# Kernel optimization log

Hardware: AMD Instinct MI355X
Metric: run time of the kernel (lower is better)

The kernel has to match this reference:

```python
import jax, jax.numpy as jnp
import numpy as np

B, C, H, W = 4, 64, 64, 64
K = C // 8  # conv_f / conv_g output channels (scale=8 since C>=8)


def setup_inputs() -> dict:
    key = jax.random.key(0)
    ks = jax.random.split(key, 8)
    x = jax.random.normal(ks[0], (B, C, H, W), dtype=jnp.float32)
    Wf = jax.random.normal(ks[1], (K, C), dtype=jnp.float32) * 0.05
    bf = jnp.zeros((K,), dtype=jnp.float32)
    Wg = jax.random.normal(ks[2], (K, C), dtype=jnp.float32) * 0.05
    bg = jnp.zeros((K,), dtype=jnp.float32)
    Wh = jax.random.normal(ks[3], (C, C), dtype=jnp.float32) * 0.05
    bh = jnp.zeros((C,), dtype=jnp.float32)
    gamma = jax.random.uniform(ks[4], (1,), dtype=jnp.float32)
    return {"x": x, "Wf": Wf, "bf": bf, "Wg": Wg, "bg": bg,
            "Wh": Wh, "bh": bh, "gamma": gamma}


def reference(x, Wf, bf, Wg, bg, Wh, bh, gamma):
    Bn, Cn, Hn, Wn = x.shape
    HW = Hn * Wn
    xf = x.reshape(Bn, Cn, HW)                               # [B, C, HW]
    # 1x1 convs == per-pixel linear maps over channels
    f = jnp.einsum('kc,bcn->bkn', Wf, xf) + bf[None, :, None]  # [B, K, HW]
    g = jnp.einsum('kc,bcn->bkn', Wg, xf) + bg[None, :, None]  # [B, K, HW]
    h = jnp.einsum('dc,bcn->bdn', Wh, xf) + bh[None, :, None]  # [B, C, HW]
    # s = f^T @ g  -> [B, HW, HW]
    s = jnp.einsum('bki,bkj->bij', f, g)
    # softmax over dim=1 (the first HW axis), matching F.softmax(s, dim=1)
    b = jax.nn.softmax(s, axis=1)
    # post-softmax lower-triangular mask applied to b^T (lower_tri=True)
    tri = jnp.tril(jnp.ones((HW, HW), dtype=x.dtype))
    b_masked = jnp.swapaxes(b, 1, 2) * tri                   # [B, HW, HW]
    o = jnp.einsum('bcn,bnm->bcm', h, b_masked)              # [B, C, HW]
    y = (gamma[0] * o + xf).reshape(Bn, Cn, Hn, Wn)
    return y
```

## Files before the change

kernel.cpp:

```cpp
#include <hip/hip_runtime.h>
#include <hip/hip_bf16.h>

#define HW 4096
#define CC 64
#define NB 4

typedef short bf16x8 __attribute__((ext_vector_type(8)));
typedef float f32x4 __attribute__((ext_vector_type(4)));

#define OFF_F  0
#define OFF_G  262144
#define OFF_H  524288
#define OFF_ZI 2621440
#define OFF_O  2686976

__device__ __forceinline__ float bf2f(short s) {
    unsigned u = ((unsigned)(unsigned short)s) << 16;
    return __uint_as_float(u);
}

__global__ __launch_bounds__(256) void k_prep(
    const float* __restrict__ x,
    const float* __restrict__ Wf, const float* __restrict__ bf,
    const float* __restrict__ Wg, const float* __restrict__ bg,
    const float* __restrict__ Wh, const float* __restrict__ bh,
    __hip_bfloat16* __restrict__ fb, __hip_bfloat16* __restrict__ gb,
    __hip_bfloat16* __restrict__ hb)
{
    __shared__ __align__(16) __hip_bfloat16 xT[64 * 72];
    __shared__ __align__(16) __hip_bfloat16 fgT[64 * 24];

    const int b  = blockIdx.y;
    const int n0 = blockIdx.x * 64;
    const int tid = (int)threadIdx.x;
    const int w = tid >> 6, lane = tid & 63, quad = lane >> 4, l15 = lane & 15;

    {
        const int n = lane;
        const float* xb = x + (size_t)b * (CC * HW) + n0 + n;
#pragma unroll
        for (int i = 0; i < 8; ++i) {
            const int c = (w + 4 * i) * 2;
            const float v0 = xb[(size_t)c * HW];
            const float v1 = xb[(size_t)(c + 1) * HW];
            __hip_bfloat16 t[2] = {__float2bfloat16(v0), __float2bfloat16(v1)};
            *reinterpret_cast<unsigned*>(&xT[n * 72 + c]) =
                *reinterpret_cast<const unsigned*>(t);
        }
    }

    bf16x8 wa[5][2];
#pragma unroll
    for (int mt = 0; mt < 5; ++mt) {
        const int row = mt * 16 + l15;
        const float* src = (row < 8) ? (Wf + row * 64)
                         : (row < 16) ? (Wg + (row - 8) * 64)
                                      : (Wh + (row - 16) * 64);
#pragma unroll
        for (int kk = 0; kk < 2; ++kk) {
            const float4 a = *(const float4*)(src + kk * 32 + quad * 8);
            const float4 c4 = *(const float4*)(src + kk * 32 + quad * 8 + 4);
            __hip_bfloat16 t[8];
            t[0] = __float2bfloat16(a.x);  t[1] = __float2bfloat16(a.y);
            t[2] = __float2bfloat16(a.z);  t[3] = __float2bfloat16(a.w);
            t[4] = __float2bfloat16(c4.x); t[5] = __float2bfloat16(c4.y);
            t[6] = __float2bfloat16(c4.z); t[7] = __float2bfloat16(c4.w);
            wa[mt][kk] = *reinterpret_cast<const bf16x8*>(t);
        }
    }

    f32x4 acc[5];
#pragma unroll
    for (int mt = 0; mt < 5; ++mt) {
#pragma unroll
        for (int r = 0; r < 4; ++r) {
            const int grow = mt * 16 + quad * 4 + r;
            acc[mt][r] = (grow < 8) ? bf[grow]
                       : (grow < 16) ? bg[grow - 8]
                                     : bh[grow - 16];
        }
    }

    __syncthreads();

    const bf16x8 b0 = *(const bf16x8*)&xT[(w * 16 + l15) * 72 + quad * 8];
    const bf16x8 b1 = *(const bf16x8*)&xT[(w * 16 + l15) * 72 + 32 + quad * 8];
#pragma unroll
    for (int mt = 0; mt < 5; ++mt) {
        acc[mt] = __builtin_amdgcn_mfma_f32_16x16x32_bf16(wa[mt][0], b0, acc[mt], 0, 0, 0);
        acc[mt] = __builtin_amdgcn_mfma_f32_16x16x32_bf16(wa[mt][1], b1, acc[mt], 0, 0, 0);
    }

#pragma unroll
    for (int mt = 1; mt < 5; ++mt) {
#pragma unroll
        for (int r = 0; r < 4; ++r) {
            const int hrow = (mt - 1) * 16 + quad * 4 + r;
            hb[((size_t)(b * 64 + hrow)) * HW + n0 + w * 16 + l15] =
                __float2bfloat16(acc[0 + mt][r]);
        }
    }

#pragma unroll
    for (int r = 0; r < 4; r += 2) {
        __hip_bfloat16 t[2] = {__float2bfloat16(acc[0][r]),
                               __float2bfloat16(acc[0][r + 1])};
        *reinterpret_cast<unsigned*>(&fgT[(w * 16 + l15) * 24 + quad * 4 + r]) =
            *reinterpret_cast<const unsigned*>(t);
    }
    __syncthreads();
    if (tid < 64) {
        const size_t bn = (size_t)b * HW + n0 + tid;
        *(float4*)(fb + bn * 8) = *(const float4*)&fgT[tid * 24];
    } else if (tid < 128) {
        const int n = tid - 64;
        const size_t bn = (size_t)b * HW + n0 + n;
        *(float4*)(gb + bn * 8) = *(const float4*)&fgT[n * 24 + 8];
    }
}

__global__ __launch_bounds__(256) void k_z(
    const __hip_bfloat16* __restrict__ fb, const __hip_bfloat16* __restrict__ gb,
    float* __restrict__ zinv)
{
    __shared__ __align__(16) __hip_bfloat16 fS[4096 * 8];
    __shared__ __align__(16) __hip_bfloat16 gS[64 * 8];
    __shared__ float zred[4][64];

    const int nt = blockIdx.x, b = blockIdx.y;
    const int n0 = nt * 64;
    const int tid = (int)threadIdx.x;
    const int w = tid >> 6, lane = tid & 63, quad = lane >> 4, l15 = lane & 15;

    const float4* fsrc = (const float4*)(fb + (size_t)b * HW * 8);
#pragma unroll
    for (int q = 0; q < 16; ++q)
        ((float4*)fS)[q * 256 + tid] = fsrc[q * 256 + tid];
    if (tid < 64)
        *(float4*)&gS[tid * 8] = *(const float4*)(gb + ((size_t)b * HW + n0 + tid) * 8);
    __syncthreads();

    const f32x4 cz = {0.f, 0.f, 0.f, 0.f};
    bf16x8 bgf[4];
#pragma unroll
    for (int ns = 0; ns < 4; ++ns) {
        bf16x8 v = {0, 0, 0, 0, 0, 0, 0, 0};
        if (quad == 0) v = *(const bf16x8*)&gS[(ns * 16 + l15) * 8];
        bgf[ns] = v;
    }

    float z[4] = {0.f, 0.f, 0.f, 0.f};
    for (int it = 0; it < 64; ++it) {
        const int i = it * 64 + w * 16;
        bf16x8 afr = {0, 0, 0, 0, 0, 0, 0, 0};
        if (quad == 0) afr = *(const bf16x8*)&fS[(i + l15) * 8];
#pragma unroll
        for (int ns = 0; ns < 4; ++ns) {
            f32x4 s = __builtin_amdgcn_mfma_f32_16x16x32_bf16(afr, bgf[ns], cz, 0, 0, 0);
            z[ns] += __expf(s[0]) + __expf(s[1]) + __expf(s[2]) + __expf(s[3]);
        }
    }

#pragma unroll
    for (int ns = 0; ns < 4; ++ns) {
        float v = z[ns];
        v += __shfl_xor(v, 16);
        v += __shfl_xor(v, 32);
        if (quad == 0) zred[w][ns * 16 + l15] = v;
    }
    __syncthreads();
    if (tid < 64) {
        float s = zred[0][tid] + zred[1][tid] + zred[2][tid] + zred[3][tid];
        zinv[(size_t)b * HW + n0 + tid] = 1.0f / s;
    }
}

__global__ __launch_bounds__(256) void k_attn(
    const __hip_bfloat16* __restrict__ fb, const __hip_bfloat16* __restrict__ gb,
    const __hip_bfloat16* __restrict__ hb, const float* __restrict__ zinv,
    __hip_bfloat16* __restrict__ opart)
{
    __shared__ __align__(16) __hip_bfloat16 gS[64 * 8];
    __shared__ __align__(16) float zS[64];
    __shared__ __align__(16) __hip_bfloat16 hT[64 * 72];
    __shared__ __align__(16) __hip_bfloat16 pT[64 * 72];

    const int hx = blockIdx.x;
    const int b  = blockIdx.y;
    const int r  = blockIdx.z;
    const int mt = (r < 32) ? r : 95 - r;
    const int m0 = mt * 64;
    const int tid = (int)threadIdx.x;
    const int w = tid >> 6, lane = tid & 63, quad = lane >> 4, l15 = lane & 15;

    const int c0s = tid >> 3,          ch0 = tid & 7;
    const int c1s = (256 + tid) >> 3,  ch1 = (256 + tid) & 7;

    const f32x4 cz = {0.f, 0.f, 0.f, 0.f};

    bf16x8 af = {0, 0, 0, 0, 0, 0, 0, 0};
    if (quad == 0)
        af = *(const bf16x8*)(fb + ((size_t)b * HW + m0 + w * 16 + l15) * 8);

    f32x4 accO[4];
#pragma unroll
    for (int i = 0; i < 4; ++i) accO[i] = cz;

    const int nc0 = mt + hx;
    float4 hv0 = make_float4(0.f, 0.f, 0.f, 0.f);
    float4 hv1 = hv0, gv = hv0, zv = hv0;
    if (nc0 < 64) {
        const int n0 = nc0 * 64;
        hv0 = *(const float4*)(hb + ((size_t)(b * 64 + c0s)) * HW + n0 + ch0 * 8);
        hv1 = *(const float4*)(hb + ((size_t)(b * 64 + c1s)) * HW + n0 + ch1 * 8);
        if (tid < 64)      gv = *(const float4*)(gb + ((size_t)b * HW + n0 + tid) * 8);
        else if (tid < 80) zv = *(const float4*)(zinv + (size_t)b * HW + n0 + (tid - 64) * 4);
    }

    for (int nc = nc0; nc < 64; nc += 4) {
        __syncthreads();
        *(float4*)&hT[c0s * 72 + ch0 * 8] = hv0;
        *(float4*)&hT[c1s * 72 + ch1 * 8] = hv1;
        if (tid < 64)      *(float4*)&gS[tid * 8] = gv;
        else if (tid < 80) *(float4*)&zS[(tid - 64) * 4] = zv;

        const int nn = nc + 4;
        if (nn < 64) {
            const int n1 = nn * 64;
            hv0 = *(const float4*)(hb + ((size_t)(b * 64 + c0s)) * HW + n1 + ch0 * 8);
            hv1 = *(const float4*)(hb + ((size_t)(b * 64 + c1s)) * HW + n1 + ch1 * 8);
            if (tid < 64)      gv = *(const float4*)(gb + ((size_t)b * HW + n1 + tid) * 8);
            else if (tid < 80) zv = *(const float4*)(zinv + (size_t)b * HW + n1 + (tid - 64) * 4);
        }
        __syncthreads();

        const int n0 = nc * 64;
        const bool diag = (nc == mt);
#pragma unroll
        for (int ns = 0; ns < 4; ++ns) {
            bf16x8 bg = {0, 0, 0, 0, 0, 0, 0, 0};
            if (quad == 0) bg = *(const bf16x8*)&gS[(ns * 16 + l15) * 8];
            f32x4 s = __builtin_amdgcn_mfma_f32_16x16x32_bf16(af, bg, cz, 0, 0, 0);
            const float zi = zS[ns * 16 + l15];
#pragma unroll
            for (int j = 0; j < 4; ++j) {
                float p = __expf(s[j]) * zi;
                if (diag) {
                    const int m = m0 + w * 16 + quad * 4 + j;
                    const int n = n0 + ns * 16 + l15;
                    if (n < m) p = 0.f;
                }
                pT[(w * 16 + quad * 4 + j) * 72 + ns * 16 + l15] = __float2bfloat16(p);
            }
        }
#pragma unroll
        for (int kb = 0; kb < 2; ++kb) {
            const bf16x8 ap =
                *(const bf16x8*)&pT[(w * 16 + l15) * 72 + kb * 32 + quad * 8];
#pragma unroll
            for (int cs = 0; cs < 4; ++cs) {
                const bf16x8 bh2 =
                    *(const bf16x8*)&hT[(cs * 16 + l15) * 72 + kb * 32 + quad * 8];
                accO[cs] = __builtin_amdgcn_mfma_f32_16x16x32_bf16(ap, bh2, accO[cs], 0, 0, 0);
            }
        }
    }

#pragma unroll
    for (int cs = 0; cs < 4; ++cs) {
        const int c = cs * 16 + l15;
        __hip_bfloat16 tmp[4];
#pragma unroll
        for (int j = 0; j < 4; ++j) tmp[j] = __float2bfloat16(accO[cs][j]);
        *(float2*)(opart + ((size_t)((hx * NB + b) * 64 + c)) * HW + m0 + w * 16 + quad * 4) =
            *(const float2*)tmp;
    }
}

__global__ __launch_bounds__(256) void k_epi(
    const __hip_bfloat16* __restrict__ opart, const float* __restrict__ x,
    const float* __restrict__ gamma, float* __restrict__ y)
{
    const int t = blockIdx.x * 256 + (int)threadIdx.x;
    const size_t e0 = (size_t)t * 8;
    const float ga = gamma[0];

    float acc[8] = {0, 0, 0, 0, 0, 0, 0, 0};
#pragma unroll
    for (int h = 0; h < 4; ++h) {
        const bf16x8 v = *(const bf16x8*)(opart + (size_t)h * (NB * CC * HW) + e0);
#pragma unroll
        for (int k = 0; k < 8; ++k) acc[k] += bf2f(v[k]);
    }
    const float4 x0 = *(const float4*)(x + e0);
    const float4 x1 = *(const float4*)(x + e0 + 4);
    float4 y0, y1;
    y0.x = ga * acc[0] + x0.x; y0.y = ga * acc[1] + x0.y;
    y0.z = ga * acc[2] + x0.z; y0.w = ga * acc[3] + x0.w;
    y1.x = ga * acc[4] + x1.x; y1.y = ga * acc[5] + x1.y;
    y1.z = ga * acc[6] + x1.z; y1.w = ga * acc[7] + x1.w;
    *(float4*)(y + e0) = y0;
    *(float4*)(y + e0 + 4) = y1;
}

extern "C" void kernel_launch(void* const* d_in, const int* in_sizes, int n_in,
                              void* d_out, int out_size, void* d_ws, size_t ws_size,
                              hipStream_t stream)
{
    const float* x     = (const float*)d_in[0];
    const float* Wf    = (const float*)d_in[1];
    const float* bf    = (const float*)d_in[2];
    const float* Wg    = (const float*)d_in[3];
    const float* bg    = (const float*)d_in[4];
    const float* Wh    = (const float*)d_in[5];
    const float* bh    = (const float*)d_in[6];
    const float* gamma = (const float*)d_in[7];

    char* ws = (char*)d_ws;
    __hip_bfloat16* fb = (__hip_bfloat16*)(ws + OFF_F);
    __hip_bfloat16* gb = (__hip_bfloat16*)(ws + OFF_G);
    __hip_bfloat16* hb = (__hip_bfloat16*)(ws + OFF_H);
    float* zinv = (float*)(ws + OFF_ZI);
    __hip_bfloat16* opart = (__hip_bfloat16*)(ws + OFF_O);
    float* y = (float*)d_out;

    k_prep<<<dim3(64, 4), 256, 0, stream>>>(x, Wf, bf, Wg, bg, Wh, bh, fb, gb, hb);
    k_z<<<dim3(64, 4), 256, 0, stream>>>(fb, gb, zinv);
    k_attn<<<dim3(4, 4, 64), 256, 0, stream>>>(fb, gb, hb, zinv, opart);
    k_epi<<<512, 256, 0, stream>>>(opart, x, gamma, y);
}
```

Baseline: 117.9 us.

## Split softmax normalizer over two row halves, halve attention column split, vectorize P stores

The normalizer kernel now splits the row range into two blocks per column tile and writes partial sums, which the attention kernel adds and inverts when staging. The attention kernel drops from four interleaved column-chunk partitions to two, and the epilogue sums two partial outputs instead of four. The score MFMA operands are swapped so each lane writes four contiguous bf16 probabilities in one vector store instead of scattered scalar stores, and the z loop prefetches the next f fragment. This raises z-kernel parallelism, cuts partial-output traffic and epilogue reads, and cuts LDS store count, but attention blocks do more sequential iterations and the grid shrinks.

Result: slower. 127.5 us (+8.1%).

```diff
diff --git a/kernel.cpp b/kernel.cpp
--- a/kernel.cpp
+++ b/kernel.cpp
@@ -6,24 +6,26 @@
 #define NB 4
 
 typedef short bf16x8 __attribute__((ext_vector_type(8)));
+typedef short bf16x4 __attribute__((ext_vector_type(4)));
 typedef float f32x4 __attribute__((ext_vector_type(4)));
 
 #define OFF_F  0
 #define OFF_G  262144
 #define OFF_H  524288
-#define OFF_ZI 2621440
-#define OFF_O  2686976
+#define OFF_ZP 2621440
+#define OFF_O  2752512
 
 __device__ __forceinline__ float bf2f(short s) {
     unsigned u = ((unsigned)(unsigned short)s) << 16;
     return __uint_as_float(u);
 }
+__device__ __forceinline__ __hip_bfloat16 f2bf(float f) { return __float2bfloat16(f); }
 
 __global__ __launch_bounds__(256) void k_prep(
     const float* __restrict__ x,
-    const float* __restrict__ Wf, const float* __restrict__ bf,
-    const float* __restrict__ Wg, const float* __restrict__ bg,
-    const float* __restrict__ Wh, const float* __restrict__ bh,
+    const float* __restrict__ Wf, const float* __restrict__ bfv,
+    const float* __restrict__ Wg, const float* __restrict__ bgv,
+    const float* __restrict__ Wh, const float* __restrict__ bhv,
     __hip_bfloat16* __restrict__ fb, __hip_bfloat16* __restrict__ gb,
     __hip_bfloat16* __restrict__ hb)
 {
@@ -43,9 +45,8 @@
             const int c = (w + 4 * i) * 2;
             const float v0 = xb[(size_t)c * HW];
             const float v1 = xb[(size_t)(c + 1) * HW];
-            __hip_bfloat16 t[2] = {__float2bfloat16(v0), __float2bfloat16(v1)};
-            *reinterpret_cast<unsigned*>(&xT[n * 72 + c]) =
-                *reinterpret_cast<const unsigned*>(t);
+            __hip_bfloat16 t[2] = {f2bf(v0), f2bf(v1)};
+            *(unsigned*)&xT[n * 72 + c] = *(const unsigned*)t;
         }
     }
 
@@ -61,11 +62,9 @@
             const float4 a = *(const float4*)(src + kk * 32 + quad * 8);
             const float4 c4 = *(const float4*)(src + kk * 32 + quad * 8 + 4);
             __hip_bfloat16 t[8];
-            t[0] = __float2bfloat16(a.x);  t[1] = __float2bfloat16(a.y);
-            t[2] = __float2bfloat16(a.z);  t[3] = __float2bfloat16(a.w);
-            t[4] = __float2bfloat16(c4.x); t[5] = __float2bfloat16(c4.y);
-            t[6] = __float2bfloat16(c4.z); t[7] = __float2bfloat16(c4.w);
-            wa[mt][kk] = *reinterpret_cast<const bf16x8*>(t);
+            t[0] = f2bf(a.x);  t[1] = f2bf(a.y);  t[2] = f2bf(a.z);  t[3] = f2bf(a.w);
+            t[4] = f2bf(c4.x); t[5] = f2bf(c4.y); t[6] = f2bf(c4.z); t[7] = f2bf(c4.w);
+            wa[mt][kk] = *(const bf16x8*)t;
         }
     }
 
@@ -75,9 +74,8 @@
 #pragma unroll
         for (int r = 0; r < 4; ++r) {
             const int grow = mt * 16 + quad * 4 + r;
-            acc[mt][r] = (grow < 8) ? bf[grow]
-                       : (grow < 16) ? bg[grow - 8]
-                                     : bh[grow - 16];
+            acc[mt][r] = (grow < 8) ? bfv[grow]
+                       : (grow < 16) ? bgv[grow - 8] : bhv[grow - 16];
         }
     }
 
@@ -96,17 +94,14 @@
 #pragma unroll
         for (int r = 0; r < 4; ++r) {
             const int hrow = (mt - 1) * 16 + quad * 4 + r;
-            hb[((size_t)(b * 64 + hrow)) * HW + n0 + w * 16 + l15] =
-                __float2bfloat16(acc[0 + mt][r]);
+            hb[((size_t)(b * 64 + hrow)) * HW + n0 + w * 16 + l15] = f2bf(acc[mt][r]);
         }
     }
 
 #pragma unroll
     for (int r = 0; r < 4; r += 2) {
-        __hip_bfloat16 t[2] = {__float2bfloat16(acc[0][r]),
-                               __float2bfloat16(acc[0][r + 1])};
-        *reinterpret_cast<unsigned*>(&fgT[(w * 16 + l15) * 24 + quad * 4 + r]) =
-            *reinterpret_cast<const unsigned*>(t);
+        __hip_bfloat16 t[2] = {f2bf(acc[0][r]), f2bf(acc[0][r + 1])};
+        *(unsigned*)&fgT[(w * 16 + l15) * 24 + quad * 4 + r] = *(const unsigned*)t;
     }
     __syncthreads();
     if (tid < 64) {
@@ -121,20 +116,20 @@
 
 __global__ __launch_bounds__(256) void k_z(
     const __hip_bfloat16* __restrict__ fb, const __hip_bfloat16* __restrict__ gb,
-    float* __restrict__ zinv)
-{
-    __shared__ __align__(16) __hip_bfloat16 fS[4096 * 8];
+    float* __restrict__ zp)
+{
+    __shared__ __align__(16) __hip_bfloat16 fS[2048 * 8];
     __shared__ __align__(16) __hip_bfloat16 gS[64 * 8];
     __shared__ float zred[4][64];
 
-    const int nt = blockIdx.x, b = blockIdx.y;
+    const int nt = blockIdx.x, b = blockIdx.y, ich = blockIdx.z;
     const int n0 = nt * 64;
     const int tid = (int)threadIdx.x;
     const int w = tid >> 6, lane = tid & 63, quad = lane >> 4, l15 = lane & 15;
 
-    const float4* fsrc = (const float4*)(fb + (size_t)b * HW * 8);
-#pragma unroll
-    for (int q = 0; q < 16; ++q)
+    const float4* fsrc = (const float4*)(fb + ((size_t)b * HW + ich * 2048) * 8);
+#pragma unroll
+    for (int q = 0; q < 8; ++q)
         ((float4*)fS)[q * 256 + tid] = fsrc[q * 256 + tid];
     if (tid < 64)
         *(float4*)&gS[tid * 8] = *(const float4*)(gb + ((size_t)b * HW + n0 + tid) * 8);
@@ -150,15 +145,18 @@
     }
 
     float z[4] = {0.f, 0.f, 0.f, 0.f};
-    for (int it = 0; it < 64; ++it) {
-        const int i = it * 64 + w * 16;
-        bf16x8 afr = {0, 0, 0, 0, 0, 0, 0, 0};
-        if (quad == 0) afr = *(const bf16x8*)&fS[(i + l15) * 8];
+    bf16x8 cur = {0, 0, 0, 0, 0, 0, 0, 0};
+    if (quad == 0) cur = *(const bf16x8*)&fS[(w * 16 + l15) * 8];
+    for (int it = 0; it < 32; ++it) {
+        bf16x8 nxt = {0, 0, 0, 0, 0, 0, 0, 0};
+        if (it + 1 < 32 && quad == 0)
+            nxt = *(const bf16x8*)&fS[((it + 1) * 64 + w * 16 + l15) * 8];
 #pragma unroll
         for (int ns = 0; ns < 4; ++ns) {
-            f32x4 s = __builtin_amdgcn_mfma_f32_16x16x32_bf16(afr, bgf[ns], cz, 0, 0, 0);
+            f32x4 s = __builtin_amdgcn_mfma_f32_16x16x32_bf16(cur, bgf[ns], cz, 0, 0, 0);
             z[ns] += __expf(s[0]) + __expf(s[1]) + __expf(s[2]) + __expf(s[3]);
         }
+        cur = nxt;
     }
 
 #pragma unroll
@@ -171,13 +169,13 @@
     __syncthreads();
     if (tid < 64) {
         float s = zred[0][tid] + zred[1][tid] + zred[2][tid] + zred[3][tid];
-        zinv[(size_t)b * HW + n0 + tid] = 1.0f / s;
+        zp[((size_t)ich * NB + b) * HW + n0 + tid] = s;
     }
 }
 
 __global__ __launch_bounds__(256) void k_attn(
     const __hip_bfloat16* __restrict__ fb, const __hip_bfloat16* __restrict__ gb,
-    const __hip_bfloat16* __restrict__ hb, const float* __restrict__ zinv,
+    const __hip_bfloat16* __restrict__ hb, const float* __restrict__ zp,
     __hip_bfloat16* __restrict__ opart)
 {
     __shared__ __align__(16) __hip_bfloat16 gS[64 * 8];
@@ -193,8 +191,8 @@
     const int tid = (int)threadIdx.x;
     const int w = tid >> 6, lane = tid & 63, quad = lane >> 4, l15 = lane & 15;
 
-    const int c0s = tid >> 3,          ch0 = tid & 7;
-    const int c1s = (256 + tid) >> 3,  ch1 = (256 + tid) & 7;
+    const int c0s = tid >> 3,         ch0 = tid & 7;
+    const int c1s = (256 + tid) >> 3, ch1 = (256 + tid) & 7;
 
     const f32x4 cz = {0.f, 0.f, 0.f, 0.f};
 
@@ -208,50 +206,66 @@
 
     const int nc0 = mt + hx;
     float4 hv0 = make_float4(0.f, 0.f, 0.f, 0.f);
-    float4 hv1 = hv0, gv = hv0, zv = hv0;
+    float4 hv1 = hv0, gv = hv0, za = hv0, zb4 = hv0;
     if (nc0 < 64) {
-        const int n0 = nc0 * 64;
-        hv0 = *(const float4*)(hb + ((size_t)(b * 64 + c0s)) * HW + n0 + ch0 * 8);
-        hv1 = *(const float4*)(hb + ((size_t)(b * 64 + c1s)) * HW + n0 + ch1 * 8);
-        if (tid < 64)      gv = *(const float4*)(gb + ((size_t)b * HW + n0 + tid) * 8);
-        else if (tid < 80) zv = *(const float4*)(zinv + (size_t)b * HW + n0 + (tid - 64) * 4);
-    }
-
-    for (int nc = nc0; nc < 64; nc += 4) {
+        const int n1 = nc0 * 64;
+        hv0 = *(const float4*)(hb + ((size_t)(b * 64 + c0s)) * HW + n1 + ch0 * 8);
+        hv1 = *(const float4*)(hb + ((size_t)(b * 64 + c1s)) * HW + n1 + ch1 * 8);
+        if (tid < 64) gv = *(const float4*)(gb + ((size_t)b * HW + n1 + tid) * 8);
+        else if (tid < 80) {
+            const int j4 = (tid - 64) * 4;
+            za  = *(const float4*)(zp + (size_t)b * HW + n1 + j4);
+            zb4 = *(const float4*)(zp + ((size_t)NB + b) * HW + n1 + j4);
+        }
+    }
+
+    for (int nc = nc0; nc < 64; nc += 2) {
         __syncthreads();
         *(float4*)&hT[c0s * 72 + ch0 * 8] = hv0;
         *(float4*)&hT[c1s * 72 + ch1 * 8] = hv1;
-        if (tid < 64)      *(float4*)&gS[tid * 8] = gv;
-        else if (tid < 80) *(float4*)&zS[(tid - 64) * 4] = zv;
-
-        const int nn = nc + 4;
+        if (tid < 64) *(float4*)&gS[tid * 8] = gv;
+        else if (tid < 80) {
+            float4 zi;
+            zi.x = 1.f / (za.x + zb4.x);
+            zi.y = 1.f / (za.y + zb4.y);
+            zi.z = 1.f / (za.z + zb4.z);
+            zi.w = 1.f / (za.w + zb4.w);
+            *(float4*)&zS[(tid - 64) * 4] = zi;
+        }
+        const int nn = nc + 2;
         if (nn < 64) {
             const int n1 = nn * 64;
             hv0 = *(const float4*)(hb + ((size_t)(b * 64 + c0s)) * HW + n1 + ch0 * 8);
             hv1 = *(const float4*)(hb + ((size_t)(b * 64 + c1s)) * HW + n1 + ch1 * 8);
-            if (tid < 64)      gv = *(const float4*)(gb + ((size_t)b * HW + n1 + tid) * 8);
-            else if (tid < 80) zv = *(const float4*)(zinv + (size_t)b * HW + n1 + (tid - 64) * 4);
+            if (tid < 64) gv = *(const float4*)(gb + ((size_t)b * HW + n1 + tid) * 8);
+            else if (tid < 80) {
+                const int j4 = (tid - 64) * 4;
+                za  = *(const float4*)(zp + (size_t)b * HW + n1 + j4);
+                zb4 = *(const float4*)(zp + ((size_t)NB + b) * HW + n1 + j4);
+            }
         }
         __syncthreads();
 
-        const int n0 = nc * 64;
+        const int n0c = nc * 64;
         const bool diag = (nc == mt);
 #pragma unroll
         for (int ns = 0; ns < 4; ++ns) {
-            bf16x8 bg = {0, 0, 0, 0, 0, 0, 0, 0};
-            if (quad == 0) bg = *(const bf16x8*)&gS[(ns * 16 + l15) * 8];
-            f32x4 s = __builtin_amdgcn_mfma_f32_16x16x32_bf16(af, bg, cz, 0, 0, 0);
-            const float zi = zS[ns * 16 + l15];
+            bf16x8 bg2 = {0, 0, 0, 0, 0, 0, 0, 0};
+            if (quad == 0) bg2 = *(const bf16x8*)&gS[(ns * 16 + l15) * 8];
+            f32x4 s = __builtin_amdgcn_mfma_f32_16x16x32_bf16(bg2, af, cz, 0, 0, 0);
+            const float4 zi4 = *(const float4*)&zS[ns * 16 + quad * 4];
+            __hip_bfloat16 t4[4];
 #pragma unroll
             for (int j = 0; j < 4; ++j) {
-                float p = __expf(s[j]) * zi;
+                float p = __expf(s[j]) * ((const float*)&zi4)[j];
                 if (diag) {
-                    const int m = m0 + w * 16 + quad * 4 + j;
-                    const int n = n0 + ns * 16 + l15;
+                    const int n = n0c + ns * 16 + quad * 4 + j;
+                    const int m = m0 + w * 16 + l15;
                     if (n < m) p = 0.f;
                 }
-                pT[(w * 16 + quad * 4 + j) * 72 + ns * 16 + l15] = __float2bfloat16(p);
+                t4[j] = f2bf(p);
             }
+            *(bf16x4*)&pT[(w * 16 + l15) * 72 + ns * 16 + quad * 4] = *(const bf16x4*)t4;
         }
 #pragma unroll
         for (int kb = 0; kb < 2; ++kb) {
@@ -271,7 +285,7 @@
         const int c = cs * 16 + l15;
         __hip_bfloat16 tmp[4];
 #pragma unroll
-        for (int j = 0; j < 4; ++j) tmp[j] = __float2bfloat16(accO[cs][j]);
+        for (int j = 0; j < 4; ++j) tmp[j] = f2bf(accO[cs][j]);
         *(float2*)(opart + ((size_t)((hx * NB + b) * 64 + c)) * HW + m0 + w * 16 + quad * 4) =
             *(const float2*)tmp;
     }
@@ -287,7 +301,7 @@
 
     float acc[8] = {0, 0, 0, 0, 0, 0, 0, 0};
 #pragma unroll
-    for (int h = 0; h < 4; ++h) {
+    for (int h = 0; h < 2; ++h) {
         const bf16x8 v = *(const bf16x8*)(opart + (size_t)h * (NB * CC * HW) + e0);
 #pragma unroll
         for (int k = 0; k < 8; ++k) acc[k] += bf2f(v[k]);
@@ -309,23 +323,23 @@
 {
     const float* x     = (const float*)d_in[0];
     const float* Wf    = (const float*)d_in[1];
-    const float* bf    = (const float*)d_in[2];
+    const float* bfv   = (const float*)d_in[2];
     const float* Wg    = (const float*)d_in[3];
-    const float* bg    = (const float*)d_in[4];
+    const float* bgv   = (const float*)d_in[4];
     const float* Wh    = (const float*)d_in[5];
-    const float* bh    = (const float*)d_in[6];
+    const float* bhv   = (const float*)d_in[6];
     const float* gamma = (const float*)d_in[7];
 
     char* ws = (char*)d_ws;
     __hip_bfloat16* fb = (__hip_bfloat16*)(ws + OFF_F);
     __hip_bfloat16* gb = (__hip_bfloat16*)(ws + OFF_G);
     __hip_bfloat16* hb = (__hip_bfloat16*)(ws + OFF_H);
-    float* zinv = (float*)(ws + OFF_ZI);
+    float* zp          = (float*)(ws + OFF_ZP);
     __hip_bfloat16* opart = (__hip_bfloat16*)(ws + OFF_O);
     float* y = (float*)d_out;
 
-    k_prep<<<dim3(64, 4), 256, 0, stream>>>(x, Wf, bf, Wg, bg, Wh, bh, fb, gb, hb);
-    k_z<<<dim3(64, 4), 256, 0, stream>>>(fb, gb, zinv);
-    k_attn<<<dim3(4, 4, 64), 256, 0, stream>>>(fb, gb, hb, zinv, opart);
+    k_prep<<<dim3(64, 4), 256, 0, stream>>>(x, Wf, bfv, Wg, bgv, Wh, bhv, fb, gb, hb);
+    k_z<<<dim3(64, 4, 2), 256, 0, stream>>>(fb, gb, zp);
+    k_attn<<<dim3(2, 4, 64), 256, 0, stream>>>(fb, gb, hb, zp, opart);
     k_epi<<<512, 256, 0, stream>>>(opart, x, gamma, y);
 }
```
